# Performance work log

Hardware: AMD Instinct MI355X
Metric: run time of the kernel (lower is better)

## Reference

```python
import jax, jax.numpy as jnp
import numpy as np

N_NODES = 65536
N_EDGES = 1048576
NODE_F = 32
EDGE_F = 8
HID = 64
OUT_F = 1
BATCH_SIZE = 64


def _glorot(key, shape):
    fan_in, fan_out = shape[0], shape[-1]
    s = jnp.sqrt(6.0 / (fan_in + fan_out))
    return jax.random.uniform(key, shape, jnp.float32, -s, s)


def setup_inputs() -> dict:
    key = jax.random.key(0)
    ks = jax.random.split(key, 20)
    inp = {
        "node_features": jax.random.normal(ks[0], (N_NODES, NODE_F), jnp.float32),
        "edge_features": jax.random.normal(ks[1], (N_EDGES, EDGE_F), jnp.float32),
        "Esrc": jax.random.randint(ks[2], (N_EDGES,), 0, N_NODES, jnp.int32),
        "Etgt": jax.random.randint(ks[3], (N_EDGES,), 0, N_NODES, jnp.int32),
        "batch": jnp.sort(jax.random.randint(ks[4], (N_NODES,), 0, BATCH_SIZE, jnp.int32)),
        # graph-conv weights
        "W_in": _glorot(ks[5], (NODE_F, HID)), "b_in": jnp.zeros((HID,), jnp.float32),
        "W_mid": _glorot(ks[6], (HID, HID)), "b_mid": jnp.zeros((HID,), jnp.float32),
        "W_out": _glorot(ks[7], (HID, OUT_F)), "b_out": jnp.zeros((OUT_F,), jnp.float32),
        # edge-encoder MLPs (Linear -> ReLU -> Linear)
        "ee_in_W1": _glorot(ks[8], (EDGE_F, HID)), "ee_in_b1": jnp.zeros((HID,), jnp.float32),
        "ee_in_W2": _glorot(ks[9], (HID, HID)), "ee_in_b2": jnp.zeros((HID,), jnp.float32),
        "ee_mid_W1": _glorot(ks[10], (EDGE_F, HID)), "ee_mid_b1": jnp.zeros((HID,), jnp.float32),
        "ee_mid_W2": _glorot(ks[11], (HID, HID)), "ee_mid_b2": jnp.zeros((HID,), jnp.float32),
        "ee_out_W1": _glorot(ks[12], (EDGE_F, OUT_F)), "ee_out_b1": jnp.zeros((OUT_F,), jnp.float32),
        "ee_out_W2": _glorot(ks[13], (OUT_F, OUT_F)), "ee_out_b2": jnp.zeros((OUT_F,), jnp.float32),
    }
    return inp


def _edge_mlp(ef, W1, b1, W2, b2):
    return jax.nn.relu(ef @ W1 + b1) @ W2 + b2  # [E, out]


def _egconv(x, W, b, Esrc, Etgt, edge_enc):
    support = x @ W                      # [N, out]
    msg = support[Esrc] * edge_enc       # [E, out] edge-gated messages
    agg = jax.ops.segment_sum(msg, Etgt, num_segments=N_NODES)  # [N, out]
    return agg + b


def reference(node_features, edge_features, Esrc, Etgt, batch,
              W_in, b_in, W_mid, b_mid, W_out, b_out,
              ee_in_W1, ee_in_b1, ee_in_W2, ee_in_b2,
              ee_mid_W1, ee_mid_b1, ee_mid_W2, ee_mid_b2,
              ee_out_W1, ee_out_b1, ee_out_W2, ee_out_b2):
    efin = _edge_mlp(edge_features, ee_in_W1, ee_in_b1, ee_in_W2, ee_in_b2)
    efmid = _edge_mlp(edge_features, ee_mid_W1, ee_mid_b1, ee_mid_W2, ee_mid_b2)
    efout = _edge_mlp(edge_features, ee_out_W1, ee_out_b1, ee_out_W2, ee_out_b2)

    x = jax.nn.relu(_egconv(node_features, W_in, b_in, Esrc, Etgt, efin))
    # dropout: identity in eval mode
    x = jax.nn.relu(_egconv(x, W_mid, b_mid, Esrc, Etgt, efmid))
    x = _egconv(x, W_out, b_out, Esrc, Etgt, efout)
    # graph-level sum pooling over batch ids
    out = jax.ops.segment_sum(x, batch, num_segments=BATCH_SIZE)  # [B, OUT_F]
    return out
```

## Files before the change

### kernel.cpp

```cpp
#include <hip/hip_runtime.h>

#define NN 65536
#define NE 1048576
#define NODE_F 32
#define EDGE_F 8
#define HID 64
#define NBATCH 64
#define NB 256
#define EPB (NE / NB)
#define NBIN 1024
#define CAP 2048
#define NREP 64

typedef __attribute__((ext_vector_type(8))) short s16x8;
typedef __attribute__((ext_vector_type(4))) float f32x4;

union FragU { s16x8 s; uint u[4]; };

__device__ inline uint pk2(float a, float b) {
    uint ua = __float_as_uint(a); ua += 0x7FFFu + ((ua >> 16) & 1u);
    uint ub = __float_as_uint(b); ub += 0x7FFFu + ((ub >> 16) & 1u);
    return (ua >> 16) | (ub & 0xFFFF0000u);
}

template<int K, bool RELUB>
__global__ __launch_bounds__(256) void node_linear(const float* __restrict__ x,
                                                   const float* __restrict__ pb,
                                                   const float* __restrict__ W,
                                                   float* __restrict__ out, int n_nodes) {
    const int lane = threadIdx.x & 63;
    const int wv = threadIdx.x >> 6;
    float wr[K];
#pragma unroll
    for (int k = 0; k < K; ++k) wr[k] = W[k * HID + lane];
    int wid = blockIdx.x * 4 + wv;
    const int nw = gridDim.x * 4;
    for (int n0 = wid; n0 < n_nodes; n0 += nw) {
        const int n = __builtin_amdgcn_readfirstlane(n0);
        const float* xr = x + (size_t)n * K;
        float acc = 0.f;
#pragma unroll
        for (int k = 0; k < K; ++k) {
            float xk = xr[k];
            if (RELUB) xk = fmaxf(xk + pb[k], 0.f);
            acc = fmaf(xk, wr[k], acc);
        }
        out[(size_t)n * HID + lane] = acc;
    }
}

__global__ __launch_bounds__(512) void p1_hist(const int* __restrict__ Etgt, int* __restrict__ bc,
                                               int* __restrict__ binTotal) {
    __shared__ int h[NBIN];
    const int blk = blockIdx.x;
    for (int t = threadIdx.x; t < NBIN; t += 512) h[t] = 0;
    __syncthreads();
    const int base = blk * EPB;
    for (int j = threadIdx.x; j < EPB; j += 512)
        atomicAdd(&h[((uint)Etgt[base + j]) >> 6], 1);
    __syncthreads();
    for (int t = threadIdx.x; t < NBIN; t += 512) {
        bc[blk * NBIN + t] = h[t];
        if (h[t]) atomicAdd(&binTotal[t], h[t]);
    }
}

__global__ __launch_bounds__(1024) void p2a_scan(const int* __restrict__ binTotal,
                                                 int* __restrict__ binStart) {
    __shared__ int part[NBIN];
    const int t = threadIdx.x;
    part[t] = binTotal[t];
    __syncthreads();
    for (int d = 1; d < NBIN; d <<= 1) {
        int v = part[t];
        int vo = (t >= d) ? part[t - d] : 0;
        __syncthreads();
        part[t] = v + vo;
        __syncthreads();
    }
    binStart[t + 1] = part[t];
    if (t == 0) binStart[0] = 0;
}

__global__ __launch_bounds__(256) void p2b_cursor(const int* __restrict__ bc,
                                                  const int* __restrict__ binStart,
                                                  int* __restrict__ cursor) {
    const int lane = threadIdx.x & 63;
    const int wv = threadIdx.x >> 6;
    const int bin = blockIdx.x * 4 + wv;
    int carry = binStart[bin];
    for (int c = 0; c < NB; c += 64) {
        const int blk = c + lane;
        const int v = bc[blk * NBIN + bin];
        int incl = v;
#pragma unroll
        for (int d = 1; d < 64; d <<= 1) {
            const int u = __shfl_up(incl, d, 64);
            if (lane >= d) incl += u;
        }
        cursor[blk * NBIN + bin] = carry + incl - v;
        carry += __shfl(incl, 63, 64);
    }
}

__global__ __launch_bounds__(512) void p3_scatter(
    const int* __restrict__ Etgt, const int* __restrict__ Esrc, const float* __restrict__ ef,
    const int* __restrict__ cursor,
    const float* __restrict__ oW1, const float* __restrict__ ob1,
    const float* __restrict__ oW2, const float* __restrict__ ob2,
    uint4* __restrict__ ef16_t, uint2* __restrict__ meta_t)
{
    __shared__ int cur[NBIN];
    const int blk = blockIdx.x;
    for (int t = threadIdx.x; t < NBIN; t += 512) cur[t] = cursor[blk * NBIN + t];
    float w[8];
#pragma unroll
    for (int k = 0; k < 8; ++k) w[k] = oW1[k];
    const float b1v = ob1[0], w2 = oW2[0], b2v = ob2[0];
    __syncthreads();
    const int base = blk * EPB;
    for (int j = threadIdx.x; j < EPB; j += 512) {
        const int i = base + j;
        const int tgt = Etgt[i];
        const int p = atomicAdd(&cur[(uint)tgt >> 6], 1);
        const float4 x = *(const float4*)(ef + (size_t)i * 8);
        const float4 y = *(const float4*)(ef + (size_t)i * 8 + 4);
        uint4 u;
        u.x = pk2(x.x, x.y); u.y = pk2(x.z, x.w);
        u.z = pk2(y.x, y.y); u.w = pk2(y.z, y.w);
        ef16_t[p] = u;
        float h = b1v;
        h = fmaf(x.x, w[0], h); h = fmaf(x.y, w[1], h);
        h = fmaf(x.z, w[2], h); h = fmaf(x.w, w[3], h);
        h = fmaf(y.x, w[4], h); h = fmaf(y.y, w[5], h);
        h = fmaf(y.z, w[6], h); h = fmaf(y.w, w[7], h);
        uint2 m;
        m.x = (uint)Esrc[i] | ((uint)tgt << 16);
        m.y = __float_as_uint(fmaxf(h, 0.f) * w2 + b2v);
        meta_t[p] = m;
    }
}

__global__ __launch_bounds__(256) void p4_sort(
    const int* __restrict__ binStart, const uint2* __restrict__ meta_t,
    const uint4* __restrict__ ef16_t,
    uint2* __restrict__ meta, uint4* __restrict__ ef16)
{
    __shared__ uint s_stp[CAP];
    __shared__ int rk[CAP];
    __shared__ int cnt[64], off[64];
    const int b = blockIdx.x;
    const int beg = binStart[b], end = binStart[b + 1];
    const int n = end - beg;
    if (threadIdx.x < 64) cnt[threadIdx.x] = 0;
    __syncthreads();
    for (int j = threadIdx.x; j < n; j += 256) {
        const uint v = meta_t[beg + j].x;
        s_stp[j] = v;
        rk[j] = atomicAdd(&cnt[(v >> 16) & 63], 1);
    }
    __syncthreads();
    if (threadIdx.x == 0) {
        int run = 0;
#pragma unroll
        for (int k = 0; k < 64; ++k) { off[k] = run; run += cnt[k]; }
    }
    __syncthreads();
    for (int j = threadIdx.x; j < n; j += 256) {
        const uint v = s_stp[j];
        const int pos = beg + off[(v >> 16) & 63] + rk[j];
        meta[pos] = meta_t[beg + j];
        ef16[pos] = ef16_t[beg + j];
    }
}

#define ISSUE(BUF, BASE_)                                                        \
    _Pragma("unroll")                                                            \
    for (int jj = 0; jj < 16; ++jj) {                                            \
        const uint stj = (uint)__builtin_amdgcn_readlane((int)st_l, (BASE_) + jj); \
        sv##BUF[jj] = support[(size_t)(stj & 0xFFFFu) * HID + lane];             \
    }

#define PROC(BUF, BASE_)                                                         \
    _Pragma("unroll")                                                            \
    for (int jj = 0; jj < 16; ++jj) {                                            \
        const int j = (BASE_) + jj;                                              \
        const int tgt = (int)((uint)__builtin_amdgcn_readlane((int)st_l, j) >> 16); \
        const ushort eu = *(const ushort*)(lds + j * 128 + ((lane * 2) ^ ((j & 7) << 4))); \
        const float ev = __uint_as_float((uint)eu << 16) + b2l;                  \
        if (tgt != tprev) {                                                      \
            float* dst = agg + (size_t)tprev * HID + lane;                       \
            if (first) { atomicAdd(dst, acc); first = 0; }                       \
            else *dst = acc;                                                     \
            acc = 0.f; tprev = tgt;                                              \
        }                                                                        \
        acc = fmaf(sv##BUF[jj], ev, acc);                                        \
    }

__global__ __launch_bounds__(256, 4) void edge_layer_fused(
    const uint4* __restrict__ ef16, const uint2* __restrict__ meta,
    const float* __restrict__ support,
    const float* __restrict__ W1, const float* __restrict__ b1,
    const float* __restrict__ W2, const float* __restrict__ b2,
    float* __restrict__ agg)
{
    __shared__ ushort lds_all[4][32 * 64];
    const int lane = threadIdx.x & 63;
    const int wv = threadIdx.x >> 6;
    char* lds = (char*)lds_all[wv];
    const int l15 = lane & 15, lhi = lane >> 4;
    const int swz = (l15 & 7) << 4;
    const float b2l = b2[lane];

    FragU a1[4];
#pragma unroll
    for (int mt = 0; mt < 4; ++mt) {
        a1[mt].u[0] = a1[mt].u[1] = a1[mt].u[2] = a1[mt].u[3] = 0;
        const int h = l15 + 16 * mt;
        if (lhi == 0) {
#pragma unroll
            for (int j = 0; j < 4; ++j)
                a1[mt].u[j] = pk2(W1[(2 * j) * HID + h], W1[(2 * j + 1) * HID + h]);
        } else if (lhi == 1) {
            a1[mt].u[0] = pk2(b1[h], 0.f);
        }
    }
    FragU a2[4][2];
#pragma unroll
    for (int mt = 0; mt < 4; ++mt)
#pragma unroll
        for (int kc = 0; kc < 2; ++kc) {
            const int o = l15 + 16 * mt;
            const int k0 = 32 * kc + 8 * lhi;
#pragma unroll
            for (int j = 0; j < 4; ++j)
                a2[mt][kc].u[j] = pk2(W2[(k0 + 2 * j) * HID + o], W2[(k0 + 2 * j + 1) * HID + o]);
        }

    for (int tile = blockIdx.x * 4 + wv; tile < NE / 32; tile += gridDim.x * 4) {
        const size_t ebase = (size_t)tile * 32;
        const uint st_l = meta[ebase + (lane & 31)].x;

#pragma unroll
        for (int nt = 0; nt < 2; ++nt) {
            FragU bf;
            bf.u[0] = bf.u[1] = bf.u[2] = bf.u[3] = 0;
            if (lhi == 0) {
                const uint4 u = ef16[ebase + nt * 16 + l15];
                bf.u[0] = u.x; bf.u[1] = u.y; bf.u[2] = u.z; bf.u[3] = u.w;
            } else if (lhi == 1) {
                bf.u[0] = 0x3F80u;
            }
            const int ebyte = (l15 + 16 * nt) * 128;
#pragma unroll
            for (int mt = 0; mt < 4; ++mt) {
                f32x4 c = {0.f, 0.f, 0.f, 0.f};
                c = __builtin_amdgcn_mfma_f32_16x16x32_bf16(a1[mt].s, bf.s, c, 0, 0, 0);
                uint2 w;
                w.x = pk2(fmaxf(c[0], 0.f), fmaxf(c[1], 0.f));
                w.y = pk2(fmaxf(c[2], 0.f), fmaxf(c[3], 0.f));
                const int hb = (16 * mt + 4 * lhi) * 2;
                *(uint2*)(lds + ebyte + (hb ^ swz)) = w;
            }
        }

        float svA[16], svB[16];
        int tprev = (int)((uint)__builtin_amdgcn_readlane((int)st_l, 0) >> 16);
        int first = 1;
        float acc = 0.f;
        ISSUE(A, 0)
        ISSUE(B, 16)

#pragma unroll
        for (int nt = 0; nt < 2; ++nt) {
            const int ebyte = (l15 + 16 * nt) * 128;
            const s16x8 bh0 = *(const s16x8*)(lds + ebyte + ((16 * lhi + 0) ^ swz));
            const s16x8 bh1 = *(const s16x8*)(lds + ebyte + ((16 * lhi + 64) ^ swz));
#pragma unroll
            for (int mt = 0; mt < 4; ++mt) {
                f32x4 c = {0.f, 0.f, 0.f, 0.f};
                c = __builtin_amdgcn_mfma_f32_16x16x32_bf16(a2[mt][0].s, bh0, c, 0, 0, 0);
                c = __builtin_amdgcn_mfma_f32_16x16x32_bf16(a2[mt][1].s, bh1, c, 0, 0, 0);
                uint2 w;
                w.x = pk2(c[0], c[1]);
                w.y = pk2(c[2], c[3]);
                const int ob = (16 * mt + 4 * lhi) * 2;
                *(uint2*)(lds + ebyte + (ob ^ swz)) = w;
            }
        }

        PROC(A, 0)
        PROC(B, 16)
        atomicAdd(agg + (size_t)tprev * HID + lane, acc);
    }
}

__global__ __launch_bounds__(256) void node_dot(const float* __restrict__ x, const float* __restrict__ pb,
                                                const float* __restrict__ w,
                                                float* __restrict__ out, int n_nodes) {
    const int lane = threadIdx.x & 63;
    const int wv = threadIdx.x >> 6;
    const float wk = w[lane];
    const float pbv = pb[lane];
    int wid = blockIdx.x * 4 + wv;
    const int nw = gridDim.x * 4;
    for (int n = wid; n < n_nodes; n += nw) {
        float v = fmaxf(x[(size_t)n * HID + lane] + pbv, 0.f) * wk;
#pragma unroll
        for (int off = 32; off >= 1; off >>= 1) v += __shfl_xor(v, off, 64);
        if (lane == 0) out[n] = v;
    }
}

__global__ __launch_bounds__(256) void edge_out_seg(
    const uint2* __restrict__ meta,
    const float* __restrict__ sup3, const int* __restrict__ batch,
    float* __restrict__ outR)
{
    const int lane = threadIdx.x & 63;
    const int wv = threadIdx.x >> 6;
    const int wid = blockIdx.x * 4 + wv;
    float* outw = outR + (size_t)(wid & (NREP - 1)) * NBATCH;
    const size_t base = (size_t)wid * 128;
    float acc = 0.f;
    int bcur = -1;
#pragma unroll
    for (int c = 0; c < 2; ++c) {
        const size_t i = base + c * 64 + lane;
        const uint2 m = meta[i];
        const float mv = sup3[m.x & 0xFFFFu] * __uint_as_float(m.y);
        const int b = batch[m.x >> 16];
        if (b != bcur) {
            if (bcur >= 0) atomicAdd(&outw[bcur], acc);
            bcur = b;
            acc = mv;
        } else {
            acc += mv;
        }
    }
    const int b0 = __builtin_amdgcn_readfirstlane(bcur);
    if (__all(bcur == b0)) {
#pragma unroll
        for (int off = 32; off >= 1; off >>= 1) acc += __shfl_xor(acc, off, 64);
        if (lane == 0) atomicAdd(&outw[b0], acc);
    } else {
        atomicAdd(&outw[bcur], acc);
    }
}

__global__ __launch_bounds__(64) void final_reduce(const float* __restrict__ outR,
                                                   float* __restrict__ out) {
    const int t = threadIdx.x;
    float s = 0.f;
#pragma unroll
    for (int r = 0; r < NREP; ++r) s += outR[r * NBATCH + t];
    atomicAdd(&out[t], s);
}

__global__ __launch_bounds__(256) void pool_bias(const int* __restrict__ batch,
                                                 const float* __restrict__ b_out,
                                                 float* __restrict__ out) {
    __shared__ int cnt[NBATCH];
    if (threadIdx.x < NBATCH) cnt[threadIdx.x] = 0;
    __syncthreads();
    const int n = blockIdx.x * 256 + threadIdx.x;
    atomicAdd(&cnt[batch[n]], 1);
    __syncthreads();
    if (threadIdx.x < NBATCH && cnt[threadIdx.x])
        atomicAdd(&out[threadIdx.x], (float)cnt[threadIdx.x] * b_out[0]);
}

extern "C" void kernel_launch(void* const* d_in, const int* in_sizes, int n_in,
                              void* d_out, int out_size, void* d_ws, size_t ws_size,
                              hipStream_t stream) {
    const float* nf    = (const float*)d_in[0];
    const float* ef    = (const float*)d_in[1];
    const int*   Esrc  = (const int*)d_in[2];
    const int*   Etgt  = (const int*)d_in[3];
    const int*   batch = (const int*)d_in[4];
    const float* W_in  = (const float*)d_in[5];
    const float* b_in  = (const float*)d_in[6];
    const float* W_mid = (const float*)d_in[7];
    const float* b_mid = (const float*)d_in[8];
    const float* W_out = (const float*)d_in[9];
    const float* b_out = (const float*)d_in[10];
    const float* eiW1  = (const float*)d_in[11];
    const float* eib1  = (const float*)d_in[12];
    const float* eiW2  = (const float*)d_in[13];
    const float* eib2  = (const float*)d_in[14];
    const float* emW1  = (const float*)d_in[15];
    const float* emb1  = (const float*)d_in[16];
    const float* emW2  = (const float*)d_in[17];
    const float* emb2  = (const float*)d_in[18];
    const float* eoW1  = (const float*)d_in[19];
    const float* eob1  = (const float*)d_in[20];
    const float* eoW2  = (const float*)d_in[21];
    const float* eob2  = (const float*)d_in[22];

    float* bufA   = (float*)d_ws;
    float* bufB   = bufA + (size_t)NN * HID;
    float* sup3   = bufB + (size_t)NN * HID;
    uint4* ef16   = (uint4*)(sup3 + NN);
    uint2* meta   = (uint2*)(ef16 + NE);
    uint4* ef16_t = (uint4*)(meta + NE);
    uint2* meta_t = (uint2*)(ef16_t + NE);
    int* bc       = (int*)(meta_t + NE);
    int* cursor   = bc + NB * NBIN;
    int* binStart = cursor + NB * NBIN;
    int* binTotal = binStart + NBIN + 1;
    float* outR   = (float*)(binTotal + NBIN);

    hipMemsetAsync(d_out, 0, NBATCH * sizeof(float), stream);
    hipMemsetAsync(binTotal, 0, NBIN * sizeof(int), stream);
    hipMemsetAsync(outR, 0, NREP * NBATCH * sizeof(float), stream);

    p1_hist<<<NB, 512, 0, stream>>>(Etgt, bc, binTotal);
    p2a_scan<<<1, 1024, 0, stream>>>(binTotal, binStart);
    p2b_cursor<<<NBIN / 4, 256, 0, stream>>>(bc, binStart, cursor);
    p3_scatter<<<NB, 512, 0, stream>>>(Etgt, Esrc, ef, cursor,
                                       eoW1, eob1, eoW2, eob2, ef16_t, meta_t);
    p4_sort<<<NBIN, 256, 0, stream>>>(binStart, meta_t, ef16_t, meta, ef16);

    node_linear<NODE_F, false><<<1024, 256, 0, stream>>>(nf, nullptr, W_in, bufA, NN);
    hipMemsetAsync(bufB, 0, (size_t)NN * HID * sizeof(float), stream);
    edge_layer_fused<<<2048, 256, 0, stream>>>(ef16, meta, bufA, eiW1, eib1, eiW2, eib2, bufB);
    node_linear<HID, true><<<1024, 256, 0, stream>>>(bufB, b_in, W_mid, bufA, NN);
    hipMemsetAsync(bufB, 0, (size_t)NN * HID * sizeof(float), stream);
    edge_layer_fused<<<2048, 256, 0, stream>>>(ef16, meta, bufA, emW1, emb1, emW2, emb2, bufB);
    node_dot<<<256, 256, 0, stream>>>(bufB, b_mid, W_out, sup3, NN);
    edge_out_seg<<<NE / 512, 256, 0, stream>>>(meta, sup3, batch, outR);
    final_reduce<<<1, 64, 0, stream>>>(outR, (float*)d_out);
    pool_bias<<<NN / 256, 256, 0, stream>>>(batch, b_out, (float*)d_out);
}
```

Baseline: 294.0 us.

## Merge scan into cursor kernel, fold final reduce into pool, widen blocks

The single-block bin-total scan kernel is removed. Each wave in the cursor kernel now computes its own exclusive prefix by summing binTotal below its bin with a wave reduction. The final_reduce kernel is folded into pool_bias, which cuts launch count by two. Histogram and scatter blocks grow to 1024 threads with fully unrolled loops, and edge_layer_fused launch bounds rise to 8 blocks per CU, which may force register spills.

```diff
diff --git a/kernel.cpp b/kernel.cpp
--- a/kernel.cpp
+++ b/kernel.cpp
@@ -49,46 +49,44 @@
     }
 }
 
-__global__ __launch_bounds__(512) void p1_hist(const int* __restrict__ Etgt, int* __restrict__ bc,
-                                               int* __restrict__ binTotal) {
+__global__ __launch_bounds__(1024) void p1_hist(const int* __restrict__ Etgt, int* __restrict__ bc,
+                                                int* __restrict__ binTotal) {
     __shared__ int h[NBIN];
     const int blk = blockIdx.x;
-    for (int t = threadIdx.x; t < NBIN; t += 512) h[t] = 0;
+    if (threadIdx.x < NBIN) h[threadIdx.x] = 0;
     __syncthreads();
     const int base = blk * EPB;
-    for (int j = threadIdx.x; j < EPB; j += 512)
-        atomicAdd(&h[((uint)Etgt[base + j]) >> 6], 1);
-    __syncthreads();
-    for (int t = threadIdx.x; t < NBIN; t += 512) {
-        bc[blk * NBIN + t] = h[t];
-        if (h[t]) atomicAdd(&binTotal[t], h[t]);
-    }
-}
-
-__global__ __launch_bounds__(1024) void p2a_scan(const int* __restrict__ binTotal,
-                                                 int* __restrict__ binStart) {
-    __shared__ int part[NBIN];
-    const int t = threadIdx.x;
-    part[t] = binTotal[t];
-    __syncthreads();
-    for (int d = 1; d < NBIN; d <<= 1) {
-        int v = part[t];
-        int vo = (t >= d) ? part[t - d] : 0;
-        __syncthreads();
-        part[t] = v + vo;
-        __syncthreads();
-    }
-    binStart[t + 1] = part[t];
-    if (t == 0) binStart[0] = 0;
-}
-
-__global__ __launch_bounds__(256) void p2b_cursor(const int* __restrict__ bc,
-                                                  const int* __restrict__ binStart,
-                                                  int* __restrict__ cursor) {
+#pragma unroll
+    for (int c = 0; c < EPB / 1024; ++c)
+        atomicAdd(&h[((uint)Etgt[base + c * 1024 + threadIdx.x]) >> 6], 1);
+    __syncthreads();
+    if (threadIdx.x < NBIN) {
+        const int v = h[threadIdx.x];
+        bc[blk * NBIN + threadIdx.x] = v;
+        if (v) atomicAdd(&binTotal[threadIdx.x], v);
+    }
+}
+
+__global__ __launch_bounds__(256) void p2_cursor(const int* __restrict__ binTotal,
+                                                 const int* __restrict__ bc,
+                                                 int* __restrict__ binStart,
+                                                 int* __restrict__ cursor) {
     const int lane = threadIdx.x & 63;
     const int wv = threadIdx.x >> 6;
     const int bin = blockIdx.x * 4 + wv;
-    int carry = binStart[bin];
+    int s = 0;
+#pragma unroll
+    for (int c = 0; c < NBIN / 64; ++c) {
+        const int t = c * 64 + lane;
+        if (t < bin) s += binTotal[t];
+    }
+#pragma unroll
+    for (int off = 32; off >= 1; off >>= 1) s += __shfl_xor(s, off, 64);
+    int carry = s;
+    if (lane == 0) {
+        binStart[bin] = carry;
+        if (bin == NBIN - 1) binStart[NBIN] = carry + binTotal[bin];
+    }
     for (int c = 0; c < NB; c += 64) {
         const int blk = c + lane;
         const int v = bc[blk * NBIN + bin];
@@ -103,7 +101,7 @@
     }
 }
 
-__global__ __launch_bounds__(512) void p3_scatter(
+__global__ __launch_bounds__(1024) void p3_scatter(
     const int* __restrict__ Etgt, const int* __restrict__ Esrc, const float* __restrict__ ef,
     const int* __restrict__ cursor,
     const float* __restrict__ oW1, const float* __restrict__ ob1,
@@ -112,15 +110,16 @@
 {
     __shared__ int cur[NBIN];
     const int blk = blockIdx.x;
-    for (int t = threadIdx.x; t < NBIN; t += 512) cur[t] = cursor[blk * NBIN + t];
+    if (threadIdx.x < NBIN) cur[threadIdx.x] = cursor[blk * NBIN + threadIdx.x];
     float w[8];
 #pragma unroll
     for (int k = 0; k < 8; ++k) w[k] = oW1[k];
     const float b1v = ob1[0], w2 = oW2[0], b2v = ob2[0];
     __syncthreads();
     const int base = blk * EPB;
-    for (int j = threadIdx.x; j < EPB; j += 512) {
-        const int i = base + j;
+#pragma unroll
+    for (int c = 0; c < EPB / 1024; ++c) {
+        const int i = base + c * 1024 + threadIdx.x;
         const int tgt = Etgt[i];
         const int p = atomicAdd(&cur[(uint)tgt >> 6], 1);
         const float4 x = *(const float4*)(ef + (size_t)i * 8);
@@ -197,7 +196,7 @@
         acc = fmaf(sv##BUF[jj], ev, acc);                                        \
     }
 
-__global__ __launch_bounds__(256, 4) void edge_layer_fused(
+__global__ __launch_bounds__(256, 8) void edge_layer_fused(
     const uint4* __restrict__ ef16, const uint2* __restrict__ meta,
     const float* __restrict__ support,
     const float* __restrict__ W1, const float* __restrict__ b1,
@@ -348,18 +347,10 @@
     }
 }
 
-__global__ __launch_bounds__(64) void final_reduce(const float* __restrict__ outR,
-                                                   float* __restrict__ out) {
-    const int t = threadIdx.x;
-    float s = 0.f;
-#pragma unroll
-    for (int r = 0; r < NREP; ++r) s += outR[r * NBATCH + t];
-    atomicAdd(&out[t], s);
-}
-
-__global__ __launch_bounds__(256) void pool_bias(const int* __restrict__ batch,
-                                                 const float* __restrict__ b_out,
-                                                 float* __restrict__ out) {
+__global__ __launch_bounds__(256) void pool_bias_final(const int* __restrict__ batch,
+                                                       const float* __restrict__ b_out,
+                                                       const float* __restrict__ outR,
+                                                       float* __restrict__ out) {
     __shared__ int cnt[NBATCH];
     if (threadIdx.x < NBATCH) cnt[threadIdx.x] = 0;
     __syncthreads();
@@ -368,6 +359,12 @@
     __syncthreads();
     if (threadIdx.x < NBATCH && cnt[threadIdx.x])
         atomicAdd(&out[threadIdx.x], (float)cnt[threadIdx.x] * b_out[0]);
+    if (blockIdx.x == 0 && threadIdx.x < NBATCH) {
+        float s = 0.f;
+#pragma unroll
+        for (int r = 0; r < NREP; ++r) s += outR[r * NBATCH + threadIdx.x];
+        atomicAdd(&out[threadIdx.x], s);
+    }
 }
 
 extern "C" void kernel_launch(void* const* d_in, const int* in_sizes, int n_in,
@@ -414,11 +411,10 @@
     hipMemsetAsync(binTotal, 0, NBIN * sizeof(int), stream);
     hipMemsetAsync(outR, 0, NREP * NBATCH * sizeof(float), stream);
 
-    p1_hist<<<NB, 512, 0, stream>>>(Etgt, bc, binTotal);
-    p2a_scan<<<1, 1024, 0, stream>>>(binTotal, binStart);
-    p2b_cursor<<<NBIN / 4, 256, 0, stream>>>(bc, binStart, cursor);
-    p3_scatter<<<NB, 512, 0, stream>>>(Etgt, Esrc, ef, cursor,
-                                       eoW1, eob1, eoW2, eob2, ef16_t, meta_t);
+    p1_hist<<<NB, 1024, 0, stream>>>(Etgt, bc, binTotal);
+    p2_cursor<<<NBIN / 4, 256, 0, stream>>>(binTotal, bc, binStart, cursor);
+    p3_scatter<<<NB, 1024, 0, stream>>>(Etgt, Esrc, ef, cursor,
+                                        eoW1, eob1, eoW2, eob2, ef16_t, meta_t);
     p4_sort<<<NBIN, 256, 0, stream>>>(binStart, meta_t, ef16_t, meta, ef16);
 
     node_linear<NODE_F, false><<<1024, 256, 0, stream>>>(nf, nullptr, W_in, bufA, NN);
@@ -429,6 +425,5 @@
     edge_layer_fused<<<2048, 256, 0, stream>>>(ef16, meta, bufA, emW1, emb1, emW2, emb2, bufB);
     node_dot<<<256, 256, 0, stream>>>(bufB, b_mid, W_out, sup3, NN);
     edge_out_seg<<<NE / 512, 256, 0, stream>>>(meta, sup3, batch, outR);
-    final_reduce<<<1, 64, 0, stream>>>(outR, (float*)d_out);
-    pool_bias<<<NN / 256, 256, 0, stream>>>(batch, b_out, (float*)d_out);
-}
+    pool_bias_final<<<NN / 256, 256, 0, stream>>>(batch, b_out, outR, (float*)d_out);
+}
```

New measurement: 593.3 us. +101.8%, slower.
